# Optimization experiments

Hardware: AMD Instinct MI355X
Metric: run time of the kernel (lower is better)

The kernel has to match this reference:

```python
import jax, jax.numpy as jnp
import numpy as np


def setup_inputs() -> dict:
    key = jax.random.key(0)
    k1, k2, k3, k4, k5 = jax.random.split(key, 5)
    B, S, IN, OUT, R = 4, 2048, 4096, 4096, 16
    x = jax.random.normal(k1, (B, S, IN), dtype=jnp.float32)
    old_weight = jax.random.normal(k2, (OUT, IN), dtype=jnp.float32) * 0.02
    old_bias = jax.random.normal(k3, (OUT,), dtype=jnp.float32) * 0.02
    lora_down = jax.random.normal(k4, (OUT, R), dtype=jnp.float32) * 0.02
    lora_up = jax.random.normal(k5, (R, IN), dtype=jnp.float32) * 0.02
    return {"x": x, "old_weight": old_weight, "old_bias": old_bias,
            "lora_down": lora_down, "lora_up": lora_up}


def reference(x, old_weight, old_bias, lora_down, lora_up):
    # weight = old_weight + lora_down @ lora_up  -> [out, in]
    # output = x @ weight.T + bias               (F.linear)
    weight = old_weight + lora_down @ lora_up
    return jnp.einsum('bsi,oi->bso', x, weight) + old_bias
```

## Files before the change

kernel.cpp:

```cpp
#include <hip/hip_runtime.h>
#include <hip/hip_bf16.h>
#include <stdint.h>


typedef __attribute__((ext_vector_type(4))) float  floatx4;
typedef __attribute__((ext_vector_type(8))) __bf16 bf16x8;

static __device__ __forceinline__ unsigned short f2bf_rne(float f) {
    union { float f; uint32_t u; } v; v.f = f;
    uint32_t r = v.u + 0x7fffu + ((v.u >> 16) & 1u);
    return (unsigned short)(r >> 16);
}

__global__ __launch_bounds__(256) void cvt_x_kernel(const float4* __restrict__ x4,
                                                    uint2* __restrict__ o2,
                                                    int n4) {
    const int stride = gridDim.x * 256;
    for (int i = blockIdx.x * 256 + threadIdx.x; i < n4; i += stride) {
        float4 a = x4[i];
        union { unsigned short s[4]; uint2 v; } o;
        o.s[0] = f2bf_rne(a.x); o.s[1] = f2bf_rne(a.y);
        o.s[2] = f2bf_rne(a.z); o.s[3] = f2bf_rne(a.w);
        o2[i] = o.v;
    }
}

#define MW_ROWS 16
__global__ __launch_bounds__(256) void merge_w_kernel(const float* __restrict__ W,
                                                      const float* __restrict__ down,
                                                      const float* __restrict__ up,
                                                      unsigned short* __restrict__ wb,
                                                      int IN) {
    const int i  = blockIdx.x * 1024 + threadIdx.x * 4;
    const int o0 = blockIdx.y * MW_ROWS;

    float4 u[16];
#pragma unroll
    for (int r = 0; r < 16; r++) u[r] = *(const float4*)(up + r * IN + i);

    for (int o = o0; o < o0 + MW_ROWS; o++) {
        float4 w = *(const float4*)(W + (size_t)o * IN + i);
#pragma unroll
        for (int r = 0; r < 16; r++) {
            const float dr = down[o * 16 + r];
            w.x += dr * u[r].x; w.y += dr * u[r].y;
            w.z += dr * u[r].z; w.w += dr * u[r].w;
        }
        union { unsigned short s[4]; uint2 v; } ov;
        ov.s[0] = f2bf_rne(w.x); ov.s[1] = f2bf_rne(w.y);
        ov.s[2] = f2bf_rne(w.z); ov.s[3] = f2bf_rne(w.w);
        *(uint2*)(wb + (size_t)o * IN + i) = ov.v;
    }
}

#define BM 256
#define BN 256
#define BK 64

static __device__ __forceinline__ void async16(const void* g, void* l) {
    auto* gp = reinterpret_cast<const __attribute__((address_space(1))) uint32_t*>(
        reinterpret_cast<uintptr_t>(g));
    auto* lp = reinterpret_cast<__attribute__((address_space(3))) uint32_t*>(
        reinterpret_cast<uintptr_t>(l));
    __builtin_amdgcn_global_load_lds(gp, lp, 16 , 0, 0);
}

__global__ __launch_bounds__(512, 2) void gemm_bt_bias_kernel(
    const unsigned short* __restrict__ A,
    const unsigned short* __restrict__ B,
    const float* __restrict__ bias,
    float* __restrict__ C,
    int M, int N, int K) {
    __shared__ __align__(16) unsigned char smem[131072];

    const int tid  = threadIdx.x;
    const int wave = tid >> 6;
    const int lane = tid & 63;
    const int wm   = wave >> 2;
    const int wn   = wave & 3;
    const int quad = lane >> 4;
    const int l16  = lane & 15;

    const int nwg = gridDim.x;
    const int bid = blockIdx.x;
    const int swz = (bid & 7) * (nwg >> 3) + (bid >> 3);
    const int ntn = N / BN;
    const int tileM = (swz / ntn) * BM;
    const int tileN = (swz % ntn) * BN;

    const int nt = K / BK;

    const int trow = tid >> 3;
    const int tcol = ((tid & 7) ^ (trow & 7)) << 3;
    const unsigned short* aG = A + (size_t)(tileM + trow) * K + tcol;
    const unsigned short* bG = B + (size_t)(tileN + trow) * K + tcol;
    unsigned char* ldst = smem + tid * 16;

#define STAGE_A(tk, h) do {                                                   \
        const size_t kof = (size_t)(((tk) & (nt - 1)) * BK);                  \
        unsigned char* d = ldst + (((tk) & 1) * 32768 + (h) * 16384);         \
        async16(aG + (size_t)((h) * 128) * K + kof, d);                       \
        async16(aG + (size_t)((h) * 128 + 64) * K + kof, d + 8192);           \
    } while (0)
#define STAGE_B(tk, h) do {                                                   \
        const size_t kof = (size_t)(((tk) & (nt - 1)) * BK);                  \
        unsigned char* d = ldst + (65536 + ((tk) & 1) * 32768 + (h) * 16384); \
        async16(bG + (size_t)((h) * 128) * K + kof, d);                       \
        async16(bG + (size_t)((h) * 128 + 64) * K + kof, d + 8192);           \
    } while (0)

    const int qs0 = ((0 * 4 + quad) ^ (l16 & 7)) * 16;
    const int qs1 = ((1 * 4 + quad) ^ (l16 & 7)) * 16;
    const int arowb = l16 * 128;
    const int browb = ((wn & 1) * 64 + l16) * 128;

    floatx4 acc[8][4];
#pragma unroll
    for (int i = 0; i < 8; i++)
#pragma unroll
        for (int j = 0; j < 4; j++) acc[i][j] = (floatx4)(0.0f);

    STAGE_A(0, 0); STAGE_A(0, 1); STAGE_B(0, 0); STAGE_B(0, 1);
    STAGE_B(1, 0); STAGE_B(1, 1);
    asm volatile("s_waitcnt vmcnt(4)" ::: "memory");
    __builtin_amdgcn_s_barrier();

#define MFMA8(mA, mB)                                                          \
    _Pragma("unroll")                                                          \
    for (int n = 0; n < 4; n++) {                                              \
        acc[mA][n] = __builtin_amdgcn_mfma_f32_16x16x32_bf16(aA0, b0[n], acc[mA][n], 0, 0, 0); \
        acc[mA][n] = __builtin_amdgcn_mfma_f32_16x16x32_bf16(aA1, b1[n], acc[mA][n], 0, 0, 0); \
        acc[mB][n] = __builtin_amdgcn_mfma_f32_16x16x32_bf16(aB0, b0[n], acc[mB][n], 0, 0, 0); \
        acc[mB][n] = __builtin_amdgcn_mfma_f32_16x16x32_bf16(aB1, b1[n], acc[mB][n], 0, 0, 0); \
    }

#pragma unroll 2
    for (int kt = 0; kt < nt; ++kt) {
        const int cur = kt & 1;
        const unsigned char* Ab = smem + (cur * 32768 + wm * 16384 + arowb);
        const unsigned char* Bb = smem + (65536 + cur * 32768 + (wn >> 1) * 16384 + browb);

        bf16x8 b0[4], b1[4];
        bf16x8 aA0, aA1, aB0, aB1;

#pragma unroll
        for (int n = 0; n < 4; n++) {
            b0[n] = *(const bf16x8*)(Bb + n * 2048 + qs0);
            b1[n] = *(const bf16x8*)(Bb + n * 2048 + qs1);
        }
        aA0 = *(const bf16x8*)(Ab + 0 * 2048 + qs0);
        aA1 = *(const bf16x8*)(Ab + 0 * 2048 + qs1);
        aB0 = *(const bf16x8*)(Ab + 1 * 2048 + qs0);
        aB1 = *(const bf16x8*)(Ab + 1 * 2048 + qs1);
        STAGE_A(kt + 1, 0);
        __builtin_amdgcn_s_barrier();
        __builtin_amdgcn_s_setprio(1);
        MFMA8(0, 1);
        __builtin_amdgcn_s_setprio(0);
        __builtin_amdgcn_s_barrier();

        aA0 = *(const bf16x8*)(Ab + 2 * 2048 + qs0);
        aA1 = *(const bf16x8*)(Ab + 2 * 2048 + qs1);
        aB0 = *(const bf16x8*)(Ab + 3 * 2048 + qs0);
        aB1 = *(const bf16x8*)(Ab + 3 * 2048 + qs1);
        STAGE_A(kt + 1, 1);
        __builtin_amdgcn_s_barrier();
        __builtin_amdgcn_s_setprio(1);
        MFMA8(2, 3);
        __builtin_amdgcn_s_setprio(0);
        __builtin_amdgcn_s_barrier();

        aA0 = *(const bf16x8*)(Ab + 4 * 2048 + qs0);
        aA1 = *(const bf16x8*)(Ab + 4 * 2048 + qs1);
        aB0 = *(const bf16x8*)(Ab + 5 * 2048 + qs0);
        aB1 = *(const bf16x8*)(Ab + 5 * 2048 + qs1);
        STAGE_B(kt + 2, 0);
        __builtin_amdgcn_s_barrier();
        __builtin_amdgcn_s_setprio(1);
        MFMA8(4, 5);
        __builtin_amdgcn_s_setprio(0);
        __builtin_amdgcn_s_barrier();

        aA0 = *(const bf16x8*)(Ab + 6 * 2048 + qs0);
        aA1 = *(const bf16x8*)(Ab + 6 * 2048 + qs1);
        aB0 = *(const bf16x8*)(Ab + 7 * 2048 + qs0);
        aB1 = *(const bf16x8*)(Ab + 7 * 2048 + qs1);
        STAGE_B(kt + 2, 1);
        __builtin_amdgcn_s_barrier();
        __builtin_amdgcn_s_setprio(1);
        MFMA8(6, 7);
        __builtin_amdgcn_s_setprio(0);
        asm volatile("s_waitcnt vmcnt(4)" ::: "memory");
        __builtin_amdgcn_s_barrier();
    }

    asm volatile("s_waitcnt vmcnt(0)" ::: "memory");

    float bv[4];
#pragma unroll
    for (int n = 0; n < 4; n++) bv[n] = bias[tileN + wn * 64 + n * 16 + l16];

#pragma unroll
    for (int m = 0; m < 8; m++) {
#pragma unroll
        for (int r = 0; r < 4; r++) {
            const int row = tileM + wm * 128 + m * 16 + quad * 4 + r;
            float* crow = C + (size_t)row * N + tileN + wn * 64 + l16;
#pragma unroll
            for (int n = 0; n < 4; n++) crow[n * 16] = acc[m][n][r] + bv[n];
        }
    }
}

extern "C" void kernel_launch(void* const* d_in, const int* in_sizes, int n_in,
                              void* d_out, int out_size, void* d_ws, size_t ws_size,
                              hipStream_t stream) {
    const float* x    = (const float*)d_in[0];
    const float* W    = (const float*)d_in[1];
    const float* bias = (const float*)d_in[2];
    const float* down = (const float*)d_in[3];
    const float* up   = (const float*)d_in[4];
    float* out = (float*)d_out;

    const int IN  = 4096;
    const int OUT = 4096;
    const int M   = in_sizes[0] / IN;

    unsigned short* xb = (unsigned short*)d_ws;
    unsigned short* wb = xb + (size_t)M * IN;

    const int n4 = M * IN / 4;
    cvt_x_kernel<<<n4 / 2 / 256, 256, 0, stream>>>((const float4*)x, (uint2*)xb, n4);
    dim3 mgrid(IN / 1024, OUT / MW_ROWS);
    merge_w_kernel<<<mgrid, 256, 0, stream>>>(W, down, up, wb, IN);

    dim3 grid((M / BM) * (OUT / BN));
    gemm_bt_bias_kernel<<<grid, 512, 0, stream>>>(xb, wb, bias, out, M, OUT, IN);
}
```

Baseline: 490.0 us.

## Switch GEMM to 32x32x16 MFMA tiles and widen x conversion stores

The GEMM inner loop now uses 32x32x16 bf16 MFMA instructions with 16-wide accumulators in place of 16x16x32. The per-wave tile stays the same but is covered by fewer, larger MFMAs, which cuts LDS fragment reads per FLOP. LDS offsets and the epilogue row mapping are reworked to match the 32x32 output layout. Separately, the x conversion kernel now packs 8 bf16 values into one 16-byte store and runs on a fixed 2048-block grid-stride launch. The new epilogue writes scattered rows, and the larger MFMAs raise register pressure.

```diff
diff --git a/kernel.cpp b/kernel.cpp
--- a/kernel.cpp
+++ b/kernel.cpp
@@ -3,8 +3,9 @@
 #include <stdint.h>
 
 
-typedef __attribute__((ext_vector_type(4))) float  floatx4;
-typedef __attribute__((ext_vector_type(8))) __bf16 bf16x8;
+typedef __attribute__((ext_vector_type(4)))  float  floatx4;
+typedef __attribute__((ext_vector_type(16))) float  floatx16;
+typedef __attribute__((ext_vector_type(8)))  __bf16 bf16x8;
 
 static __device__ __forceinline__ unsigned short f2bf_rne(float f) {
     union { float f; uint32_t u; } v; v.f = f;
@@ -13,15 +14,18 @@
 }
 
 __global__ __launch_bounds__(256) void cvt_x_kernel(const float4* __restrict__ x4,
-                                                    uint2* __restrict__ o2,
-                                                    int n4) {
+                                                    uint4* __restrict__ o4,
+                                                    int n8) {
     const int stride = gridDim.x * 256;
-    for (int i = blockIdx.x * 256 + threadIdx.x; i < n4; i += stride) {
-        float4 a = x4[i];
-        union { unsigned short s[4]; uint2 v; } o;
+    for (int i = blockIdx.x * 256 + threadIdx.x; i < n8; i += stride) {
+        float4 a = x4[2 * i];
+        float4 b = x4[2 * i + 1];
+        union { unsigned short s[8]; uint4 v; } o;
         o.s[0] = f2bf_rne(a.x); o.s[1] = f2bf_rne(a.y);
         o.s[2] = f2bf_rne(a.z); o.s[3] = f2bf_rne(a.w);
-        o2[i] = o.v;
+        o.s[4] = f2bf_rne(b.x); o.s[5] = f2bf_rne(b.y);
+        o.s[6] = f2bf_rne(b.z); o.s[7] = f2bf_rne(b.w);
+        o4[i] = o.v;
     }
 }
 
@@ -78,8 +82,8 @@
     const int lane = tid & 63;
     const int wm   = wave >> 2;
     const int wn   = wave & 3;
-    const int quad = lane >> 4;
-    const int l16  = lane & 15;
+    const int l5   = lane & 31;
+    const int lhi  = lane >> 5;
 
     const int nwg = gridDim.x;
     const int bid = blockIdx.x;
@@ -109,30 +113,43 @@
         async16(bG + (size_t)((h) * 128 + 64) * K + kof, d + 8192);           \
     } while (0)
 
-    const int qs0 = ((0 * 4 + quad) ^ (l16 & 7)) * 16;
-    const int qs1 = ((1 * 4 + quad) ^ (l16 & 7)) * 16;
-    const int arowb = l16 * 128;
-    const int browb = ((wn & 1) * 64 + l16) * 128;
-
-    floatx4 acc[8][4];
-#pragma unroll
-    for (int i = 0; i < 8; i++)
-#pragma unroll
-        for (int j = 0; j < 4; j++) acc[i][j] = (floatx4)(0.0f);
+    const int gk  = l5 & 7;
+    const int qs0 = ((0 + lhi) ^ gk) << 4;
+    const int qs1 = ((2 + lhi) ^ gk) << 4;
+    const int qs2 = ((4 + lhi) ^ gk) << 4;
+    const int qs3 = ((6 + lhi) ^ gk) << 4;
+    const int arowb = l5 * 128;
+    const int browb = ((wn & 1) * 64 + l5) * 128;
+
+    floatx16 acc[4][2];
+#pragma unroll
+    for (int i = 0; i < 4; i++) {
+        acc[i][0] = (floatx16)(0.0f);
+        acc[i][1] = (floatx16)(0.0f);
+    }
 
     STAGE_A(0, 0); STAGE_A(0, 1); STAGE_B(0, 0); STAGE_B(0, 1);
     STAGE_B(1, 0); STAGE_B(1, 1);
     asm volatile("s_waitcnt vmcnt(4)" ::: "memory");
     __builtin_amdgcn_s_barrier();
 
-#define MFMA8(mA, mB)                                                          \
-    _Pragma("unroll")                                                          \
-    for (int n = 0; n < 4; n++) {                                              \
-        acc[mA][n] = __builtin_amdgcn_mfma_f32_16x16x32_bf16(aA0, b0[n], acc[mA][n], 0, 0, 0); \
-        acc[mA][n] = __builtin_amdgcn_mfma_f32_16x16x32_bf16(aA1, b1[n], acc[mA][n], 0, 0, 0); \
-        acc[mB][n] = __builtin_amdgcn_mfma_f32_16x16x32_bf16(aB0, b0[n], acc[mB][n], 0, 0, 0); \
-        acc[mB][n] = __builtin_amdgcn_mfma_f32_16x16x32_bf16(aB1, b1[n], acc[mB][n], 0, 0, 0); \
-    }
+#define MFMA_PHASE(bm)                                                         \
+    do {                                                                       \
+        acc[bm][0] = __builtin_amdgcn_mfma_f32_32x32x16_bf16(a0, bf00, acc[bm][0], 0, 0, 0); \
+        acc[bm][1] = __builtin_amdgcn_mfma_f32_32x32x16_bf16(a0, bf10, acc[bm][1], 0, 0, 0); \
+        acc[bm][0] = __builtin_amdgcn_mfma_f32_32x32x16_bf16(a1, bf01, acc[bm][0], 0, 0, 0); \
+        acc[bm][1] = __builtin_amdgcn_mfma_f32_32x32x16_bf16(a1, bf11, acc[bm][1], 0, 0, 0); \
+        acc[bm][0] = __builtin_amdgcn_mfma_f32_32x32x16_bf16(a2, bf02, acc[bm][0], 0, 0, 0); \
+        acc[bm][1] = __builtin_amdgcn_mfma_f32_32x32x16_bf16(a2, bf12, acc[bm][1], 0, 0, 0); \
+        acc[bm][0] = __builtin_amdgcn_mfma_f32_32x32x16_bf16(a3, bf03, acc[bm][0], 0, 0, 0); \
+        acc[bm][1] = __builtin_amdgcn_mfma_f32_32x32x16_bf16(a3, bf13, acc[bm][1], 0, 0, 0); \
+    } while (0)
+
+#define LOAD_A(bm)                                                             \
+        a0 = *(const bf16x8*)(Ab + (bm) * 4096 + qs0);                         \
+        a1 = *(const bf16x8*)(Ab + (bm) * 4096 + qs1);                         \
+        a2 = *(const bf16x8*)(Ab + (bm) * 4096 + qs2);                         \
+        a3 = *(const bf16x8*)(Ab + (bm) * 4096 + qs3)
 
 #pragma unroll 2
     for (int kt = 0; kt < nt; ++kt) {
@@ -140,55 +157,46 @@
         const unsigned char* Ab = smem + (cur * 32768 + wm * 16384 + arowb);
         const unsigned char* Bb = smem + (65536 + cur * 32768 + (wn >> 1) * 16384 + browb);
 
-        bf16x8 b0[4], b1[4];
-        bf16x8 aA0, aA1, aB0, aB1;
-
-#pragma unroll
-        for (int n = 0; n < 4; n++) {
-            b0[n] = *(const bf16x8*)(Bb + n * 2048 + qs0);
-            b1[n] = *(const bf16x8*)(Bb + n * 2048 + qs1);
-        }
-        aA0 = *(const bf16x8*)(Ab + 0 * 2048 + qs0);
-        aA1 = *(const bf16x8*)(Ab + 0 * 2048 + qs1);
-        aB0 = *(const bf16x8*)(Ab + 1 * 2048 + qs0);
-        aB1 = *(const bf16x8*)(Ab + 1 * 2048 + qs1);
+        bf16x8 bf00, bf01, bf02, bf03, bf10, bf11, bf12, bf13;
+        bf16x8 a0, a1, a2, a3;
+
+        bf00 = *(const bf16x8*)(Bb + 0 * 4096 + qs0);
+        bf01 = *(const bf16x8*)(Bb + 0 * 4096 + qs1);
+        bf02 = *(const bf16x8*)(Bb + 0 * 4096 + qs2);
+        bf03 = *(const bf16x8*)(Bb + 0 * 4096 + qs3);
+        bf10 = *(const bf16x8*)(Bb + 1 * 4096 + qs0);
+        bf11 = *(const bf16x8*)(Bb + 1 * 4096 + qs1);
+        bf12 = *(const bf16x8*)(Bb + 1 * 4096 + qs2);
+        bf13 = *(const bf16x8*)(Bb + 1 * 4096 + qs3);
+        LOAD_A(0);
         STAGE_A(kt + 1, 0);
         __builtin_amdgcn_s_barrier();
         __builtin_amdgcn_s_setprio(1);
-        MFMA8(0, 1);
-        __builtin_amdgcn_s_setprio(0);
-        __builtin_amdgcn_s_barrier();
-
-        aA0 = *(const bf16x8*)(Ab + 2 * 2048 + qs0);
-        aA1 = *(const bf16x8*)(Ab + 2 * 2048 + qs1);
-        aB0 = *(const bf16x8*)(Ab + 3 * 2048 + qs0);
-        aB1 = *(const bf16x8*)(Ab + 3 * 2048 + qs1);
+        MFMA_PHASE(0);
+        __builtin_amdgcn_s_setprio(0);
+        __builtin_amdgcn_s_barrier();
+
+        LOAD_A(1);
         STAGE_A(kt + 1, 1);
         __builtin_amdgcn_s_barrier();
         __builtin_amdgcn_s_setprio(1);
-        MFMA8(2, 3);
-        __builtin_amdgcn_s_setprio(0);
-        __builtin_amdgcn_s_barrier();
-
-        aA0 = *(const bf16x8*)(Ab + 4 * 2048 + qs0);
-        aA1 = *(const bf16x8*)(Ab + 4 * 2048 + qs1);
-        aB0 = *(const bf16x8*)(Ab + 5 * 2048 + qs0);
-        aB1 = *(const bf16x8*)(Ab + 5 * 2048 + qs1);
+        MFMA_PHASE(1);
+        __builtin_amdgcn_s_setprio(0);
+        __builtin_amdgcn_s_barrier();
+
+        LOAD_A(2);
         STAGE_B(kt + 2, 0);
         __builtin_amdgcn_s_barrier();
         __builtin_amdgcn_s_setprio(1);
-        MFMA8(4, 5);
-        __builtin_amdgcn_s_setprio(0);
-        __builtin_amdgcn_s_barrier();
-
-        aA0 = *(const bf16x8*)(Ab + 6 * 2048 + qs0);
-        aA1 = *(const bf16x8*)(Ab + 6 * 2048 + qs1);
-        aB0 = *(const bf16x8*)(Ab + 7 * 2048 + qs0);
-        aB1 = *(const bf16x8*)(Ab + 7 * 2048 + qs1);
+        MFMA_PHASE(2);
+        __builtin_amdgcn_s_setprio(0);
+        __builtin_amdgcn_s_barrier();
+
+        LOAD_A(3);
         STAGE_B(kt + 2, 1);
         __builtin_amdgcn_s_barrier();
         __builtin_amdgcn_s_setprio(1);
-        MFMA8(6, 7);
+        MFMA_PHASE(3);
         __builtin_amdgcn_s_setprio(0);
         asm volatile("s_waitcnt vmcnt(4)" ::: "memory");
         __builtin_amdgcn_s_barrier();
@@ -196,18 +204,17 @@
 
     asm volatile("s_waitcnt vmcnt(0)" ::: "memory");
 
-    float bv[4];
-#pragma unroll
-    for (int n = 0; n < 4; n++) bv[n] = bias[tileN + wn * 64 + n * 16 + l16];
-
-#pragma unroll
-    for (int m = 0; m < 8; m++) {
-#pragma unroll
-        for (int r = 0; r < 4; r++) {
-            const int row = tileM + wm * 128 + m * 16 + quad * 4 + r;
-            float* crow = C + (size_t)row * N + tileN + wn * 64 + l16;
-#pragma unroll
-            for (int n = 0; n < 4; n++) crow[n * 16] = acc[m][n][r] + bv[n];
+    const float bv0 = bias[tileN + wn * 64 + l5];
+    const float bv1 = bias[tileN + wn * 64 + 32 + l5];
+
+#pragma unroll
+    for (int bm = 0; bm < 4; bm++) {
+#pragma unroll
+        for (int r = 0; r < 16; r++) {
+            const int row = tileM + wm * 128 + bm * 32 + (r & 3) + ((r >> 2) << 3) + (lhi << 2);
+            float* crow = C + (size_t)row * N + tileN + wn * 64 + l5;
+            crow[0]  = acc[bm][0][r] + bv0;
+            crow[32] = acc[bm][1][r] + bv1;
         }
     }
 }
@@ -229,8 +236,8 @@
     unsigned short* xb = (unsigned short*)d_ws;
     unsigned short* wb = xb + (size_t)M * IN;
 
-    const int n4 = M * IN / 4;
-    cvt_x_kernel<<<n4 / 2 / 256, 256, 0, stream>>>((const float4*)x, (uint2*)xb, n4);
+    const int n8 = M * IN / 8;
+    cvt_x_kernel<<<2048, 256, 0, stream>>>((const float4*)x, (uint4*)xb, n8);
     dim3 mgrid(IN / 1024, OUT / MW_ROWS);
     merge_w_kernel<<<mgrid, 256, 0, stream>>>(W, down, up, wb, IN);
 
```

Result: slower. 526.0 us (+7.4%).
